# Performance work log

Hardware: AMD Instinct MI355X
Metric: run time of the kernel (lower is better)

## Reference

```python
import jax, jax.numpy as jnp
import numpy as np

N = 50000      # nodes
E = 800000     # edges
XS = 64        # x_size
ES = 32        # edge_attr dim (in_size = XS + ES = 96)
OUT = 64       # out_size
H = 128        # hidden_size
EPS = 1e-5


def _lin_init(k, fan_in, fan_out):
    s = 1.0 / np.sqrt(fan_in)
    kw, kb = jax.random.split(k)
    w = jax.random.uniform(kw, (fan_in, fan_out), minval=-s, maxval=s, dtype=jnp.float32)
    b = jax.random.uniform(kb, (fan_out,), minval=-s, maxval=s, dtype=jnp.float32)
    return w, b


def setup_inputs() -> dict:
    key = jax.random.key(0)
    ks = jax.random.split(key, 12)
    x = jax.random.normal(ks[0], (N, XS), dtype=jnp.float32)
    edge_index = jax.random.randint(ks[1], (2, E), 0, N, dtype=jnp.int64)
    edge_attr = jax.random.normal(ks[2], (E, ES), dtype=jnp.float32)
    u = jax.random.normal(ks[3], (1, 8), dtype=jnp.float32)
    batch = jnp.zeros((N,), dtype=jnp.int64)
    # MLP1: (96->128) LReLU (128->128) LReLU (128->64) LReLU LN(64)
    m1w0, m1b0 = _lin_init(ks[4], XS + ES, H)
    m1w1, m1b1 = _lin_init(ks[5], H, H)
    m1w2, m1b2 = _lin_init(ks[6], H, OUT)
    ln1_g = jnp.ones((OUT,), jnp.float32); ln1_b = jnp.zeros((OUT,), jnp.float32)
    # MLP2: (128->128) LReLU (128->128) LReLU (128->64) LReLU LN(64)
    m2w0, m2b0 = _lin_init(ks[7], XS + OUT, H)
    m2w1, m2b1 = _lin_init(ks[8], H, H)
    m2w2, m2b2 = _lin_init(ks[9], H, OUT)
    ln2_g = jnp.ones((OUT,), jnp.float32); ln2_b = jnp.zeros((OUT,), jnp.float32)
    return dict(x=x, edge_index=edge_index, edge_attr=edge_attr, u=u, batch=batch,
                m1w0=m1w0, m1b0=m1b0, m1w1=m1w1, m1b1=m1b1, m1w2=m1w2, m1b2=m1b2,
                ln1_g=ln1_g, ln1_b=ln1_b,
                m2w0=m2w0, m2b0=m2b0, m2w1=m2w1, m2b1=m2b1, m2w2=m2w2, m2b2=m2b2,
                ln2_g=ln2_g, ln2_b=ln2_b)


def _lrelu(v):
    return jax.nn.leaky_relu(v, 0.01)


def _layernorm(v, g, b):
    mu = jnp.mean(v, axis=-1, keepdims=True)
    var = jnp.mean(jnp.square(v - mu), axis=-1, keepdims=True)
    return (v - mu) * jax.lax.rsqrt(var + EPS) * g + b


def _mlp(h, w0, b0, w1, b1, w2, b2, g, bn):
    h = _lrelu(h @ w0 + b0)
    h = _lrelu(h @ w1 + b1)
    h = _lrelu(h @ w2 + b2)          # activate_last=True
    return _layernorm(h, g, bn)      # layer_norm=True


def reference(x, edge_index, edge_attr, u, batch,
              m1w0, m1b0, m1w1, m1b1, m1w2, m1b2, ln1_g, ln1_b,
              m2w0, m2b0, m2w1, m2b1, m2w2, m2b2, ln2_g, ln2_b):
    row, col = edge_index[0], edge_index[1]
    # gather source nodes, concat edge features -> per-edge MLP
    h = jnp.concatenate([x[row], edge_attr], axis=1)            # [E, 96]
    h = _mlp(h, m1w0, m1b0, m1w1, m1b1, m1w2, m1b2, ln1_g, ln1_b)  # [E, 64]
    # scatter_mean over destination nodes
    agg = jax.ops.segment_sum(h, col, num_segments=N)           # [N, 64]
    cnt = jax.ops.segment_sum(jnp.ones((E,), h.dtype), col, num_segments=N)
    agg = agg / jnp.maximum(cnt, 1.0)[:, None]
    # node update MLP
    h2 = jnp.concatenate([x, agg], axis=1)                      # [N, 128]
    return _mlp(h2, m2w0, m2b0, m2w1, m2b1, m2w2, m2b2, ln2_g, ln2_b)
```

## Files before the change

kernel.cpp:

```cpp
#include <hip/hip_runtime.h>


#define NNODES 50000
#define NEDGES 800000
#define NTILES_E2 3125
#define NTILES_N2 196

typedef __bf16 bf16;
typedef __bf16 __attribute__((ext_vector_type(4))) bf16x4;
typedef __bf16 __attribute__((ext_vector_type(8))) bf16x8;
typedef float __attribute__((ext_vector_type(4))) f32x4;

__device__ __forceinline__ f32x4 mfma_bf16(bf16x8 a, bf16x8 b, f32x4 c) {
    return __builtin_amdgcn_mfma_f32_16x16x32_bf16(a, b, c, 0, 0, 0);
}

__global__ void prep_weights(const float* __restrict__ w10, const float* __restrict__ w11,
                             const float* __restrict__ w12, const float* __restrict__ w20,
                             const float* __restrict__ w21, const float* __restrict__ w22,
                             bf16* __restrict__ img) {
    int idx = blockIdx.x * 256 + threadIdx.x;
    float f;
    if (idx < 13312) {
        int n = idx / 104, k = idx % 104;
        f = (k < 96) ? w10[k * 128 + n] : 0.0f;
    } else if (idx < 30720) {
        int t = idx - 13312; int n = t / 136, k = t % 136;
        f = (k < 128) ? w11[k * 128 + n] : 0.0f;
    } else if (idx < 39424) {
        int t = idx - 30720; int n = t / 136, k = t % 136;
        f = (k < 128) ? w12[k * 64 + n] : 0.0f;
    } else if (idx < 56832) {
        int t = idx - 39424; int n = t / 136, k = t % 136;
        f = (k < 128) ? w20[k * 128 + n] : 0.0f;
    } else if (idx < 74240) {
        int t = idx - 56832; int n = t / 136, k = t % 136;
        f = (k < 128) ? w21[k * 128 + n] : 0.0f;
    } else if (idx < 82944) {
        int t = idx - 74240; int n = t / 136, k = t % 136;
        f = (k < 128) ? w22[k * 64 + n] : 0.0f;
    } else {
        return;
    }
    img[idx] = (bf16)f;
}

__global__ void hist_kernel(const int* __restrict__ col, int* __restrict__ hist) {
    int i = blockIdx.x * 512 + threadIdx.x;
    if (i < NEDGES) {
        int d = col[i];
        if ((unsigned)d < (unsigned)NNODES) atomicAdd(hist + d, 1);
    }
}

__global__ void scanA(const int* __restrict__ hist, int* __restrict__ off,
                      int* __restrict__ csum) {
    __shared__ int sd[512];
    int t = threadIdx.x, i = blockIdx.x * 512 + t;
    int v = (i < NNODES) ? hist[i] : 0;
    sd[t] = v;
    __syncthreads();
    for (int o2 = 1; o2 < 512; o2 <<= 1) {
        int x = (t >= o2) ? sd[t - o2] : 0;
        __syncthreads();
        sd[t] += x;
        __syncthreads();
    }
    if (i < NNODES) off[i] = sd[t] - v;
    if (t == 511) csum[blockIdx.x] = sd[511];
}

__global__ void scanB(int* __restrict__ csum) {
    __shared__ int sd[128];
    int t = threadIdx.x;
    int v = (t < 98) ? csum[t] : 0;
    sd[t] = v;
    __syncthreads();
    for (int o2 = 1; o2 < 128; o2 <<= 1) {
        int x = (t >= o2) ? sd[t - o2] : 0;
        __syncthreads();
        sd[t] += x;
        __syncthreads();
    }
    if (t < 98) csum[t] = sd[t] - v;
}

__global__ void scanC(int* __restrict__ off, const int* __restrict__ csum) {
    int i = blockIdx.x * 512 + threadIdx.x;
    if (i < NNODES) off[i] += csum[blockIdx.x];
}

__global__ void scatter_kernel(const int* __restrict__ eidx, int* __restrict__ off,
                               int* __restrict__ perm, int* __restrict__ rdS) {
    int i = blockIdx.x * 512 + threadIdx.x;
    if (i < NEDGES) {
        int r = eidx[i], d = eidx[NEDGES + i];
        if ((unsigned)d < (unsigned)NNODES && (unsigned)r < (unsigned)NNODES) {
            int pos = atomicAdd(off + d, 1);
            if ((unsigned)pos < (unsigned)NEDGES) {
                perm[pos] = i;
                rdS[pos] = (int)(((unsigned)r & 0xFFFFu) | ((unsigned)d << 16));
            }
        }
    }
}

__global__ __launch_bounds__(512, 2) void edge_mlp(
    const float* __restrict__ x, const int* __restrict__ perm,
    const int* __restrict__ rdS, const float* __restrict__ eattr,
    const bf16* __restrict__ wimg,
    const float* __restrict__ b0g, const float* __restrict__ b1g,
    const float* __restrict__ b2g, const float* __restrict__ lng,
    const float* __restrict__ lnb, float* __restrict__ agg) {
    __shared__ __align__(16) bf16 wall[39424];
    __shared__ __align__(16) bf16 buf[256 * 136];
    __shared__ float bs[448];
    __shared__ int dstile[256];

    const int tid = threadIdx.x;
    {
        const uint4* src = (const uint4*)wimg;
        uint4* dst = (uint4*)wall;
        for (int i = tid; i < 4928; i += 512) dst[i] = src[i];
    }
    if (tid < 128) { bs[tid] = b0g[tid]; bs[128 + tid] = b1g[tid]; }
    else if (tid < 192) {
        int t = tid - 128;
        bs[256 + t] = b2g[t]; bs[320 + t] = lng[t]; bs[384 + t] = lnb[t];
    }
    __syncthreads();

    const int lane = tid & 63;
    const int wv = tid >> 6;
    const int col16 = lane & 15;
    const int quad = lane >> 4;

    float b0r[8], b1r[8], b2r[4], gr[4], br[4];
#pragma unroll
    for (int i = 0; i < 8; i++) { b0r[i] = bs[i * 16 + col16]; b1r[i] = bs[128 + i * 16 + col16]; }
#pragma unroll
    for (int i = 0; i < 4; i++) {
        b2r[i] = bs[256 + i * 16 + col16];
        gr[i] = bs[320 + i * 16 + col16];
        br[i] = bs[384 + i * 16 + col16];
    }

    const bf16* w0t = wall;
    const bf16* w1t = wall + 13312;
    const bf16* w2t = wall + 30720;

    const f32x4 vzero = {0.0f, 0.0f, 0.0f, 0.0f};
    const int r0 = wv * 32 + col16;
    const int rw = wv * 32 + quad * 4;
    const int el = tid >> 1, half = tid & 1;
    const int G = gridDim.x;

    int tile = blockIdx.x;

    float4 xr[8], er[4];
    unsigned cv;
    {
        int s = tile * 256 + el;
        cv = (unsigned)rdS[s];
        int ce = perm[s];
        int r = (int)(cv & 0xFFFFu); if (r >= NNODES) r = 0;
        if ((unsigned)ce >= (unsigned)NEDGES) ce = 0;
        const float4* xs = (const float4*)(x + (size_t)r * 64) + half * 8;
        const float4* es = (const float4*)(eattr + (size_t)ce * 32) + half * 4;
#pragma unroll
        for (int j = 0; j < 8; j++) xr[j] = xs[j];
#pragma unroll
        for (int j = 0; j < 4; j++) er[j] = es[j];
    }
    unsigned nv; int ne;
    {
        int t1 = tile + G;
        int s = (t1 < NTILES_E2 ? t1 * 256 : 0) + el;
        nv = (unsigned)rdS[s];
        ne = perm[s];
    }

    for (; tile < NTILES_E2; tile += G) {
        {
            unsigned d = cv >> 16;
            if (half == 0) dstile[el] = (d < (unsigned)NNODES) ? (int)d : 0;
            bf16* arow = buf + el * 136;
#pragma unroll
            for (int j = 0; j < 8; j++) {
                float4 vv = xr[j];
                bf16x4 u = {(bf16)vv.x, (bf16)vv.y, (bf16)vv.z, (bf16)vv.w};
                *(bf16x4*)(arow + half * 32 + j * 4) = u;
            }
#pragma unroll
            for (int j = 0; j < 4; j++) {
                float4 vv = er[j];
                bf16x4 u = {(bf16)vv.x, (bf16)vv.y, (bf16)vv.z, (bf16)vv.w};
                *(bf16x4*)(arow + 64 + half * 16 + j * 4) = u;
            }
        }
        __syncthreads();

        {
            int t2 = tile + G;
            if (t2 < NTILES_E2) {
                int r = (int)(nv & 0xFFFFu); if (r >= NNODES) r = 0;
                int e = ne; if ((unsigned)e >= (unsigned)NEDGES) e = 0;
                const float4* xs = (const float4*)(x + (size_t)r * 64) + half * 8;
                const float4* es = (const float4*)(eattr + (size_t)e * 32) + half * 4;
#pragma unroll
                for (int j = 0; j < 8; j++) xr[j] = xs[j];
#pragma unroll
                for (int j = 0; j < 4; j++) er[j] = es[j];
            }
        }
        unsigned pv; int pe;
        {
            int t3 = tile + 2 * G;
            int s = (t3 < NTILES_E2 ? t3 * 256 : 0) + el;
            pv = (unsigned)rdS[s];
            pe = perm[s];
        }

        f32x4 acc1[2][8];
#pragma unroll
        for (int mt = 0; mt < 2; mt++)
#pragma unroll
            for (int nt = 0; nt < 8; nt++) acc1[mt][nt] = vzero;
#pragma unroll
        for (int ks = 0; ks < 3; ks++) {
            bf16x8 a0 = *(const bf16x8*)(buf + r0 * 136 + ks * 32 + quad * 8);
            bf16x8 a1 = *(const bf16x8*)(buf + (r0 + 16) * 136 + ks * 32 + quad * 8);
#pragma unroll
            for (int nt = 0; nt < 8; nt++) {
                bf16x8 b = *(const bf16x8*)(w0t + (nt * 16 + col16) * 104 + ks * 32 + quad * 8);
                acc1[0][nt] = mfma_bf16(a0, b, acc1[0][nt]);
                acc1[1][nt] = mfma_bf16(a1, b, acc1[1][nt]);
            }
        }
#pragma unroll
        for (int mt = 0; mt < 2; mt++)
#pragma unroll
            for (int nt = 0; nt < 8; nt++)
#pragma unroll
                for (int rg = 0; rg < 4; rg++) {
                    float v = acc1[mt][nt][rg] + b0r[nt];
                    v = (v > 0.0f) ? v : 0.01f * v;
                    buf[(rw + mt * 16 + rg) * 136 + nt * 16 + col16] = (bf16)v;
                }

        bf16x8 a2[2][4];
#pragma unroll
        for (int mt = 0; mt < 2; mt++)
#pragma unroll
            for (int ks = 0; ks < 4; ks++)
                a2[mt][ks] = *(const bf16x8*)(buf + (r0 + mt * 16) * 136 + ks * 32 + quad * 8);
        f32x4 acc2[2][8];
#pragma unroll
        for (int mt = 0; mt < 2; mt++)
#pragma unroll
            for (int nt = 0; nt < 8; nt++) acc2[mt][nt] = vzero;
#pragma unroll
        for (int ks = 0; ks < 4; ks++) {
#pragma unroll
            for (int nt = 0; nt < 8; nt++) {
                bf16x8 b = *(const bf16x8*)(w1t + (nt * 16 + col16) * 136 + ks * 32 + quad * 8);
                acc2[0][nt] = mfma_bf16(a2[0][ks], b, acc2[0][nt]);
                acc2[1][nt] = mfma_bf16(a2[1][ks], b, acc2[1][nt]);
            }
        }
#pragma unroll
        for (int mt = 0; mt < 2; mt++)
#pragma unroll
            for (int nt = 0; nt < 8; nt++)
#pragma unroll
                for (int rg = 0; rg < 4; rg++) {
                    float v = acc2[mt][nt][rg] + b1r[nt];
                    v = (v > 0.0f) ? v : 0.01f * v;
                    buf[(rw + mt * 16 + rg) * 136 + nt * 16 + col16] = (bf16)v;
                }

        bf16x8 a3[2][4];
#pragma unroll
        for (int mt = 0; mt < 2; mt++)
#pragma unroll
            for (int ks = 0; ks < 4; ks++)
                a3[mt][ks] = *(const bf16x8*)(buf + (r0 + mt * 16) * 136 + ks * 32 + quad * 8);
        f32x4 acc3[2][4];
#pragma unroll
        for (int mt = 0; mt < 2; mt++)
#pragma unroll
            for (int nt = 0; nt < 4; nt++) acc3[mt][nt] = vzero;
#pragma unroll
        for (int ks = 0; ks < 4; ks++) {
#pragma unroll
            for (int nt = 0; nt < 4; nt++) {
                bf16x8 b = *(const bf16x8*)(w2t + (nt * 16 + col16) * 136 + ks * 32 + quad * 8);
                acc3[0][nt] = mfma_bf16(a3[0][ks], b, acc3[0][nt]);
                acc3[1][nt] = mfma_bf16(a3[1][ks], b, acc3[1][nt]);
            }
        }

        int drA[2][4];
#pragma unroll
        for (int mt = 0; mt < 2; mt++)
#pragma unroll
            for (int rg = 0; rg < 4; rg++) {
                int c = dstile[rw + mt * 16 + rg];
                drA[mt][rg] = ((unsigned)c < (unsigned)NNODES) ? c : 0;
            }
        __syncthreads();

#pragma unroll
        for (int mt = 0; mt < 2; mt++) {
            float vals[4][4];
            float s1[4] = {0.f, 0.f, 0.f, 0.f}, s2[4] = {0.f, 0.f, 0.f, 0.f};
#pragma unroll
            for (int nt = 0; nt < 4; nt++)
#pragma unroll
                for (int rg = 0; rg < 4; rg++) {
                    float v = acc3[mt][nt][rg] + b2r[nt];
                    v = (v > 0.0f) ? v : 0.01f * v;
                    vals[nt][rg] = v;
                    s1[rg] += v;
                    s2[rg] += v * v;
                }
#pragma unroll
            for (int off2 = 1; off2 < 16; off2 <<= 1) {
#pragma unroll
                for (int rg = 0; rg < 4; rg++) {
                    s1[rg] += __shfl_xor(s1[rg], off2);
                    s2[rg] += __shfl_xor(s2[rg], off2);
                }
            }
            float o[4][4];
#pragma unroll
            for (int rg = 0; rg < 4; rg++) {
                float mu = s1[rg] * 0.015625f;
                float var = s2[rg] * 0.015625f - mu * mu;
                float rstd = rsqrtf(var + 1e-5f);
#pragma unroll
                for (int nt = 0; nt < 4; nt++)
                    o[nt][rg] = (vals[nt][rg] - mu) * rstd * gr[nt] + br[nt];
            }
            float run0 = o[0][0], run1 = o[1][0], run2 = o[2][0], run3 = o[3][0];
            int cur = drA[mt][0];
#pragma unroll
            for (int rg = 1; rg < 4; rg++) {
                if (drA[mt][rg] != cur) {
                    float* dst = agg + (size_t)cur * 64 + col16;
                    atomicAdd(dst, run0); atomicAdd(dst + 16, run1);
                    atomicAdd(dst + 32, run2); atomicAdd(dst + 48, run3);
                    run0 = o[0][rg]; run1 = o[1][rg]; run2 = o[2][rg]; run3 = o[3][rg];
                    cur = drA[mt][rg];
                } else {
                    run0 += o[0][rg]; run1 += o[1][rg]; run2 += o[2][rg]; run3 += o[3][rg];
                }
            }
            float* dst = agg + (size_t)cur * 64 + col16;
            atomicAdd(dst, run0); atomicAdd(dst + 16, run1);
            atomicAdd(dst + 32, run2); atomicAdd(dst + 48, run3);
        }

        cv = nv; nv = pv; ne = pe;
    }
}

__global__ __launch_bounds__(512, 2) void node_mlp(
    const float* __restrict__ x, const float* __restrict__ agg,
    const int* __restrict__ hist, const bf16* __restrict__ wimg,
    const float* __restrict__ b0g, const float* __restrict__ b1g,
    const float* __restrict__ b2g, const float* __restrict__ lng,
    const float* __restrict__ lnb, float* __restrict__ out) {
    __shared__ __align__(16) bf16 wall[43520];
    __shared__ __align__(16) bf16 buf[256 * 136];
    __shared__ float bs[448];

    const int tid = threadIdx.x;
    {
        const uint4* src = (const uint4*)wimg;
        uint4* dst = (uint4*)wall;
        for (int i = tid; i < 5440; i += 512) dst[i] = src[i];
    }
    if (tid < 128) { bs[tid] = b0g[tid]; bs[128 + tid] = b1g[tid]; }
    else if (tid < 192) {
        int t = tid - 128;
        bs[256 + t] = b2g[t]; bs[320 + t] = lng[t]; bs[384 + t] = lnb[t];
    }
    __syncthreads();

    const int lane = tid & 63;
    const int wv = tid >> 6;
    const int col16 = lane & 15;
    const int quad = lane >> 4;

    float b0r[8], b1r[8], b2r[4], gr[4], br[4];
#pragma unroll
    for (int i = 0; i < 8; i++) { b0r[i] = bs[i * 16 + col16]; b1r[i] = bs[128 + i * 16 + col16]; }
#pragma unroll
    for (int i = 0; i < 4; i++) {
        b2r[i] = bs[256 + i * 16 + col16];
        gr[i] = bs[320 + i * 16 + col16];
        br[i] = bs[384 + i * 16 + col16];
    }

    const bf16* w0t = wall;
    const bf16* w1t = wall + 17408;
    const bf16* w2t = wall + 34816;

    const f32x4 vzero = {0.0f, 0.0f, 0.0f, 0.0f};
    const int r0 = wv * 32 + col16;
    const int rw = wv * 32 + quad * 4;
    const int el = tid >> 1, half = tid & 1;
    const int G = gridDim.x;

    int tile = blockIdx.x;
    if (tile >= NTILES_N2) return;

    float4 xr[8], ar[8];
    int cc;
    {
        int i = tile * 256 + el;
        if (i >= NNODES) i = NNODES - 1;
        const float4* xs = (const float4*)(x + (size_t)i * 64) + half * 8;
        const float4* as = (const float4*)(agg + (size_t)i * 64) + half * 8;
#pragma unroll
        for (int j = 0; j < 8; j++) { xr[j] = xs[j]; ar[j] = as[j]; }
        cc = hist[i];
    }

    for (; tile < NTILES_N2; tile += G) {
        const int nbase = tile * 256;
        {
            float inv = 1.0f / (float)(cc > 1 ? cc : 1);
            bf16* arow = buf + el * 136;
#pragma unroll
            for (int j = 0; j < 8; j++) {
                float4 v = xr[j];
                bf16x4 u = {(bf16)v.x, (bf16)v.y, (bf16)v.z, (bf16)v.w};
                *(bf16x4*)(arow + half * 32 + j * 4) = u;
            }
#pragma unroll
            for (int j = 0; j < 8; j++) {
                float4 v = ar[j];
                bf16x4 u = {(bf16)(v.x * inv), (bf16)(v.y * inv), (bf16)(v.z * inv), (bf16)(v.w * inv)};
                *(bf16x4*)(arow + 64 + half * 32 + j * 4) = u;
            }
        }
        __syncthreads();

        {
            int t2 = tile + G;
            if (t2 < NTILES_N2) {
                int i = t2 * 256 + el;
                if (i >= NNODES) i = NNODES - 1;
                const float4* xs = (const float4*)(x + (size_t)i * 64) + half * 8;
                const float4* as = (const float4*)(agg + (size_t)i * 64) + half * 8;
#pragma unroll
                for (int j = 0; j < 8; j++) { xr[j] = xs[j]; ar[j] = as[j]; }
                cc = hist[i];
            }
        }

        f32x4 acc1[2][8];
#pragma unroll
        for (int mt = 0; mt < 2; mt++)
#pragma unroll
            for (int nt = 0; nt < 8; nt++) acc1[mt][nt] = vzero;
#pragma unroll
        for (int ks = 0; ks < 4; ks++) {
            bf16x8 a0 = *(const bf16x8*)(buf + r0 * 136 + ks * 32 + quad * 8);
            bf16x8 a1 = *(const bf16x8*)(buf + (r0 + 16) * 136 + ks * 32 + quad * 8);
#pragma unroll
            for (int nt = 0; nt < 8; nt++) {
                bf16x8 b = *(const bf16x8*)(w0t + (nt * 16 + col16) * 136 + ks * 32 + quad * 8);
                acc1[0][nt] = mfma_bf16(a0, b, acc1[0][nt]);
                acc1[1][nt] = mfma_bf16(a1, b, acc1[1][nt]);
            }
        }
#pragma unroll
        for (int mt = 0; mt < 2; mt++)
#pragma unroll
            for (int nt = 0; nt < 8; nt++)
#pragma unroll
                for (int rg = 0; rg < 4; rg++) {
                    float v = acc1[mt][nt][rg] + b0r[nt];
                    v = (v > 0.0f) ? v : 0.01f * v;
                    buf[(rw + mt * 16 + rg) * 136 + nt * 16 + col16] = (bf16)v;
                }

        bf16x8 a2[2][4];
#pragma unroll
        for (int mt = 0; mt < 2; mt++)
#pragma unroll
            for (int ks = 0; ks < 4; ks++)
                a2[mt][ks] = *(const bf16x8*)(buf + (r0 + mt * 16) * 136 + ks * 32 + quad * 8);
        f32x4 acc2[2][8];
#pragma unroll
        for (int mt = 0; mt < 2; mt++)
#pragma unroll
            for (int nt = 0; nt < 8; nt++) acc2[mt][nt] = vzero;
#pragma unroll
        for (int ks = 0; ks < 4; ks++) {
#pragma unroll
            for (int nt = 0; nt < 8; nt++) {
                bf16x8 b = *(const bf16x8*)(w1t + (nt * 16 + col16) * 136 + ks * 32 + quad * 8);
                acc2[0][nt] = mfma_bf16(a2[0][ks], b, acc2[0][nt]);
                acc2[1][nt] = mfma_bf16(a2[1][ks], b, acc2[1][nt]);
            }
        }
#pragma unroll
        for (int mt = 0; mt < 2; mt++)
#pragma unroll
            for (int nt = 0; nt < 8; nt++)
#pragma unroll
                for (int rg = 0; rg < 4; rg++) {
                    float v = acc2[mt][nt][rg] + b1r[nt];
                    v = (v > 0.0f) ? v : 0.01f * v;
                    buf[(rw + mt * 16 + rg) * 136 + nt * 16 + col16] = (bf16)v;
                }

        bf16x8 a3[2][4];
#pragma unroll
        for (int mt = 0; mt < 2; mt++)
#pragma unroll
            for (int ks = 0; ks < 4; ks++)
                a3[mt][ks] = *(const bf16x8*)(buf + (r0 + mt * 16) * 136 + ks * 32 + quad * 8);
        f32x4 acc3[2][4];
#pragma unroll
        for (int mt = 0; mt < 2; mt++)
#pragma unroll
            for (int nt = 0; nt < 4; nt++) acc3[mt][nt] = vzero;
#pragma unroll
        for (int ks = 0; ks < 4; ks++) {
#pragma unroll
            for (int nt = 0; nt < 4; nt++) {
                bf16x8 b = *(const bf16x8*)(w2t + (nt * 16 + col16) * 136 + ks * 32 + quad * 8);
                acc3[0][nt] = mfma_bf16(a3[0][ks], b, acc3[0][nt]);
                acc3[1][nt] = mfma_bf16(a3[1][ks], b, acc3[1][nt]);
            }
        }
        __syncthreads();

#pragma unroll
        for (int mt = 0; mt < 2; mt++) {
            float vals[4][4];
            float s1[4] = {0.f, 0.f, 0.f, 0.f}, s2[4] = {0.f, 0.f, 0.f, 0.f};
#pragma unroll
            for (int nt = 0; nt < 4; nt++)
#pragma unroll
                for (int rg = 0; rg < 4; rg++) {
                    float v = acc3[mt][nt][rg] + b2r[nt];
                    v = (v > 0.0f) ? v : 0.01f * v;
                    vals[nt][rg] = v;
                    s1[rg] += v;
                    s2[rg] += v * v;
                }
#pragma unroll
            for (int off2 = 1; off2 < 16; off2 <<= 1) {
#pragma unroll
                for (int rg = 0; rg < 4; rg++) {
                    s1[rg] += __shfl_xor(s1[rg], off2);
                    s2[rg] += __shfl_xor(s2[rg], off2);
                }
            }
#pragma unroll
            for (int rg = 0; rg < 4; rg++) {
                float mu = s1[rg] * 0.015625f;
                float var = s2[rg] * 0.015625f - mu * mu;
                float rstd = rsqrtf(var + 1e-5f);
                int i = nbase + rw + mt * 16 + rg;
                if (i < NNODES) {
#pragma unroll
                    for (int nt = 0; nt < 4; nt++) {
                        float o = (vals[nt][rg] - mu) * rstd * gr[nt] + br[nt];
                        out[(size_t)i * 64 + nt * 16 + col16] = o;
                    }
                }
            }
        }
    }
}

extern "C" void kernel_launch(void* const* d_in, const int* in_sizes, int n_in,
                              void* d_out, int out_size, void* d_ws, size_t ws_size,
                              hipStream_t stream) {
    (void)in_sizes; (void)n_in; (void)out_size; (void)ws_size;
    const float* x     = (const float*)d_in[0];
    const int*   eidx  = (const int*)d_in[1];
    const float* eattr = (const float*)d_in[2];
    const float* m1w0 = (const float*)d_in[5];
    const float* m1b0 = (const float*)d_in[6];
    const float* m1w1 = (const float*)d_in[7];
    const float* m1b1 = (const float*)d_in[8];
    const float* m1w2 = (const float*)d_in[9];
    const float* m1b2 = (const float*)d_in[10];
    const float* ln1g = (const float*)d_in[11];
    const float* ln1b = (const float*)d_in[12];
    const float* m2w0 = (const float*)d_in[13];
    const float* m2b0 = (const float*)d_in[14];
    const float* m2w1 = (const float*)d_in[15];
    const float* m2b1 = (const float*)d_in[16];
    const float* m2w2 = (const float*)d_in[17];
    const float* m2b2 = (const float*)d_in[18];
    const float* ln2g = (const float*)d_in[19];
    const float* ln2b = (const float*)d_in[20];

    char* ws = (char*)d_ws;
    float* agg  = (float*)ws;
    int*   hist = (int*)(ws + 12800000);
    int*   off  = (int*)(ws + 13000000);
    int*   csum = (int*)(ws + 13200000);
    int*   perm = (int*)(ws + 13200512);
    int*   rdS  = (int*)(ws + 16400512);
    bf16*  wimg = (bf16*)(ws + 19600512);

    hipMemsetAsync(d_ws, 0, 13000000, stream);
    prep_weights<<<324, 256, 0, stream>>>(m1w0, m1w1, m1w2, m2w0, m2w1, m2w2, wimg);
    hist_kernel<<<1563, 512, 0, stream>>>(eidx + NEDGES, hist);
    scanA<<<98, 512, 0, stream>>>(hist, off, csum);
    scanB<<<1, 128, 0, stream>>>(csum);
    scanC<<<98, 512, 0, stream>>>(off, csum);
    scatter_kernel<<<1563, 512, 0, stream>>>(eidx, off, perm, rdS);
    edge_mlp<<<256, 512, 0, stream>>>(x, perm, rdS, eattr, wimg, m1b0, m1b1, m1b2,
                                      ln1g, ln1b, agg);
    node_mlp<<<196, 512, 0, stream>>>(x, agg, hist, wimg + 39424,
                                      m2b0, m2b1, m2b2, ln2g, ln2b, (float*)d_out);
}
```

Before: 489.6 us.

## Fuse all stages into one persistent cooperative kernel with grid syncs

Replaces the memset, weight prep, histogram, three-stage scan, scatter, edge MLP and node MLP launches with a single cooperative kernel of 256 blocks that separates phases with grid-wide syncs. Zeroing and weight conversion now run inside the kernel, and the scan's second pass is replaced by each block summing the preceding block totals. This removes per-launch overhead and gaps between the many small kernels. In exchange it adds several grid barriers, runs the small phases with only 256 blocks, and the node MLP must now share one larger LDS allocation and launch configuration with the edge phase.

New measurement: 942.3 us. 92.5% more time.

```diff
diff --git a/kernel.cpp b/kernel.cpp
--- a/kernel.cpp
+++ b/kernel.cpp
@@ -1,10 +1,15 @@
 #include <hip/hip_runtime.h>
+#include <hip/hip_cooperative_groups.h>
+
+namespace cg = cooperative_groups;
 
 
 #define NNODES 50000
 #define NEDGES 800000
-#define NTILES_E2 3125
-#define NTILES_N2 196
+#define NTILES_E 3125
+#define NTILES_N 196
+#define GRID 256
+#define TPB 512
 
 typedef __bf16 bf16;
 typedef __bf16 __attribute__((ext_vector_type(4))) bf16x4;
@@ -15,85 +20,104 @@
     return __builtin_amdgcn_mfma_f32_16x16x32_bf16(a, b, c, 0, 0, 0);
 }
 
-__global__ void prep_weights(const float* __restrict__ w10, const float* __restrict__ w11,
-                             const float* __restrict__ w12, const float* __restrict__ w20,
-                             const float* __restrict__ w21, const float* __restrict__ w22,
-                             bf16* __restrict__ img) {
-    int idx = blockIdx.x * 256 + threadIdx.x;
-    float f;
-    if (idx < 13312) {
-        int n = idx / 104, k = idx % 104;
-        f = (k < 96) ? w10[k * 128 + n] : 0.0f;
-    } else if (idx < 30720) {
-        int t = idx - 13312; int n = t / 136, k = t % 136;
-        f = (k < 128) ? w11[k * 128 + n] : 0.0f;
-    } else if (idx < 39424) {
-        int t = idx - 30720; int n = t / 136, k = t % 136;
-        f = (k < 128) ? w12[k * 64 + n] : 0.0f;
-    } else if (idx < 56832) {
-        int t = idx - 39424; int n = t / 136, k = t % 136;
-        f = (k < 128) ? w20[k * 128 + n] : 0.0f;
-    } else if (idx < 74240) {
-        int t = idx - 56832; int n = t / 136, k = t % 136;
-        f = (k < 128) ? w21[k * 128 + n] : 0.0f;
-    } else if (idx < 82944) {
-        int t = idx - 74240; int n = t / 136, k = t % 136;
-        f = (k < 128) ? w22[k * 64 + n] : 0.0f;
-    } else {
-        return;
-    }
-    img[idx] = (bf16)f;
-}
-
-__global__ void hist_kernel(const int* __restrict__ col, int* __restrict__ hist) {
-    int i = blockIdx.x * 512 + threadIdx.x;
-    if (i < NEDGES) {
-        int d = col[i];
+__global__ __launch_bounds__(TPB) void fused_gnn(
+    const float* __restrict__ x, const int* __restrict__ eidx,
+    const float* __restrict__ eattr,
+    const float* __restrict__ w10, const float* __restrict__ w11,
+    const float* __restrict__ w12, const float* __restrict__ w20,
+    const float* __restrict__ w21, const float* __restrict__ w22,
+    const float* __restrict__ b10, const float* __restrict__ b11,
+    const float* __restrict__ b12, const float* __restrict__ l1g,
+    const float* __restrict__ l1b,
+    const float* __restrict__ b20, const float* __restrict__ b21,
+    const float* __restrict__ b22, const float* __restrict__ l2g,
+    const float* __restrict__ l2b,
+    float* __restrict__ out, char* __restrict__ ws) {
+    cg::grid_group gg = cg::this_grid();
+
+    float* agg  = (float*)ws;
+    int*   hist = (int*)(ws + 12800000);
+    int*   off  = (int*)(ws + 13000000);
+    int*   csum = (int*)(ws + 13200000);
+    int*   perm = (int*)(ws + 13200512);
+    int*   rdS  = (int*)(ws + 16400512);
+    bf16*  wimg = (bf16*)(ws + 19600512);
+
+    __shared__ __align__(16) bf16 wall[43520];
+    __shared__ __align__(16) bf16 buf[256 * 136];
+    __shared__ float bs[448];
+    __shared__ int dstile[256];
+
+    const int tid = threadIdx.x;
+    const int gtid = blockIdx.x * TPB + tid;
+    const int gstride = GRID * TPB;
+
+    for (int i = gtid; i < 3250000; i += gstride) ((int*)ws)[i] = 0;
+    for (int idx = gtid; idx < 82944; idx += gstride) {
+        float f;
+        if (idx < 13312)      { int n = idx / 104, k = idx % 104; f = (k < 96) ? w10[k * 128 + n] : 0.0f; }
+        else if (idx < 30720) { int t2 = idx - 13312; int n = t2 / 136, k = t2 % 136; f = (k < 128) ? w11[k * 128 + n] : 0.0f; }
+        else if (idx < 39424) { int t2 = idx - 30720; int n = t2 / 136, k = t2 % 136; f = (k < 128) ? w12[k * 64 + n] : 0.0f; }
+        else if (idx < 56832) { int t2 = idx - 39424; int n = t2 / 136, k = t2 % 136; f = (k < 128) ? w20[k * 128 + n] : 0.0f; }
+        else if (idx < 74240) { int t2 = idx - 56832; int n = t2 / 136, k = t2 % 136; f = (k < 128) ? w21[k * 128 + n] : 0.0f; }
+        else                  { int t2 = idx - 74240; int n = t2 / 136, k = t2 % 136; f = (k < 128) ? w22[k * 64 + n] : 0.0f; }
+        wimg[idx] = (bf16)f;
+    }
+    __threadfence();
+    gg.sync();
+
+    {
+        const uint4* src = (const uint4*)wimg;
+        uint4* dst = (uint4*)wall;
+        for (int i = tid; i < 4928; i += TPB) dst[i] = src[i];
+    }
+    if (tid < 128) { bs[tid] = b10[tid]; bs[128 + tid] = b11[tid]; }
+    else if (tid < 192) {
+        int t2 = tid - 128;
+        bs[256 + t2] = b12[t2]; bs[320 + t2] = l1g[t2]; bs[384 + t2] = l1b[t2];
+    }
+    for (int i = gtid; i < NEDGES; i += gstride) {
+        int d = eidx[NEDGES + i];
         if ((unsigned)d < (unsigned)NNODES) atomicAdd(hist + d, 1);
     }
-}
-
-__global__ void scanA(const int* __restrict__ hist, int* __restrict__ off,
-                      int* __restrict__ csum) {
-    __shared__ int sd[512];
-    int t = threadIdx.x, i = blockIdx.x * 512 + t;
-    int v = (i < NNODES) ? hist[i] : 0;
-    sd[t] = v;
-    __syncthreads();
-    for (int o2 = 1; o2 < 512; o2 <<= 1) {
-        int x = (t >= o2) ? sd[t - o2] : 0;
+    __threadfence();
+    gg.sync();
+
+    if (blockIdx.x < 98) {
+        int* sd = (int*)buf;
+        int i = blockIdx.x * 512 + tid;
+        int v = (i < NNODES) ? hist[i] : 0;
+        sd[tid] = v;
         __syncthreads();
-        sd[t] += x;
+        for (int o2 = 1; o2 < 512; o2 <<= 1) {
+            int xv = (tid >= o2) ? sd[tid - o2] : 0;
+            __syncthreads();
+            sd[tid] += xv;
+            __syncthreads();
+        }
+        if (i < NNODES) off[i] = sd[tid] - v;
+        if (tid == 511) csum[blockIdx.x] = sd[511];
+    }
+    __threadfence();
+    gg.sync();
+
+    if (blockIdx.x < 98) {
+        if (tid < 64) {
+            int p = 0;
+            for (int j = tid; j < (int)blockIdx.x; j += 64) p += csum[j];
+#pragma unroll
+            for (int o = 32; o > 0; o >>= 1) p += __shfl_down(p, o);
+            if (tid == 0) dstile[0] = p;
+        }
         __syncthreads();
-    }
-    if (i < NNODES) off[i] = sd[t] - v;
-    if (t == 511) csum[blockIdx.x] = sd[511];
-}
-
-__global__ void scanB(int* __restrict__ csum) {
-    __shared__ int sd[128];
-    int t = threadIdx.x;
-    int v = (t < 98) ? csum[t] : 0;
-    sd[t] = v;
-    __syncthreads();
-    for (int o2 = 1; o2 < 128; o2 <<= 1) {
-        int x = (t >= o2) ? sd[t - o2] : 0;
-        __syncthreads();
-        sd[t] += x;
-        __syncthreads();
-    }
-    if (t < 98) csum[t] = sd[t] - v;
-}
-
-__global__ void scanC(int* __restrict__ off, const int* __restrict__ csum) {
-    int i = blockIdx.x * 512 + threadIdx.x;
-    if (i < NNODES) off[i] += csum[blockIdx.x];
-}
-
-__global__ void scatter_kernel(const int* __restrict__ eidx, int* __restrict__ off,
-                               int* __restrict__ perm, int* __restrict__ rdS) {
-    int i = blockIdx.x * 512 + threadIdx.x;
-    if (i < NEDGES) {
+        int pre = dstile[0];
+        int i = blockIdx.x * 512 + tid;
+        if (i < NNODES) off[i] += pre;
+    }
+    __threadfence();
+    gg.sync();
+
+    for (int i = gtid; i < NEDGES; i += gstride) {
         int r = eidx[i], d = eidx[NEDGES + i];
         if ((unsigned)d < (unsigned)NNODES && (unsigned)r < (unsigned)NNODES) {
             int pos = atomicAdd(off + d, 1);
@@ -103,477 +127,408 @@
             }
         }
     }
-}
-
-__global__ __launch_bounds__(512, 2) void edge_mlp(
-    const float* __restrict__ x, const int* __restrict__ perm,
-    const int* __restrict__ rdS, const float* __restrict__ eattr,
-    const bf16* __restrict__ wimg,
-    const float* __restrict__ b0g, const float* __restrict__ b1g,
-    const float* __restrict__ b2g, const float* __restrict__ lng,
-    const float* __restrict__ lnb, float* __restrict__ agg) {
-    __shared__ __align__(16) bf16 wall[39424];
-    __shared__ __align__(16) bf16 buf[256 * 136];
-    __shared__ float bs[448];
-    __shared__ int dstile[256];
-
-    const int tid = threadIdx.x;
-    {
-        const uint4* src = (const uint4*)wimg;
-        uint4* dst = (uint4*)wall;
-        for (int i = tid; i < 4928; i += 512) dst[i] = src[i];
-    }
-    if (tid < 128) { bs[tid] = b0g[tid]; bs[128 + tid] = b1g[tid]; }
-    else if (tid < 192) {
-        int t = tid - 128;
-        bs[256 + t] = b2g[t]; bs[320 + t] = lng[t]; bs[384 + t] = lnb[t];
-    }
-    __syncthreads();
+    __threadfence();
+    gg.sync();
 
     const int lane = tid & 63;
     const int wv = tid >> 6;
     const int col16 = lane & 15;
     const int quad = lane >> 4;
-
-    float b0r[8], b1r[8], b2r[4], gr[4], br[4];
-#pragma unroll
-    for (int i = 0; i < 8; i++) { b0r[i] = bs[i * 16 + col16]; b1r[i] = bs[128 + i * 16 + col16]; }
-#pragma unroll
-    for (int i = 0; i < 4; i++) {
-        b2r[i] = bs[256 + i * 16 + col16];
-        gr[i] = bs[320 + i * 16 + col16];
-        br[i] = bs[384 + i * 16 + col16];
-    }
-
-    const bf16* w0t = wall;
-    const bf16* w1t = wall + 13312;
-    const bf16* w2t = wall + 30720;
-
+    const int el = tid >> 1, half = tid & 1;
     const f32x4 vzero = {0.0f, 0.0f, 0.0f, 0.0f};
-    const int r0 = wv * 32 + col16;
-    const int rw = wv * 32 + quad * 4;
-    const int el = tid >> 1, half = tid & 1;
-    const int G = gridDim.x;
-
-    int tile = blockIdx.x;
-
-    float4 xr[8], er[4];
-    unsigned cv;
     {
-        int s = tile * 256 + el;
-        cv = (unsigned)rdS[s];
-        int ce = perm[s];
-        int r = (int)(cv & 0xFFFFu); if (r >= NNODES) r = 0;
-        if ((unsigned)ce >= (unsigned)NEDGES) ce = 0;
-        const float4* xs = (const float4*)(x + (size_t)r * 64) + half * 8;
-        const float4* es = (const float4*)(eattr + (size_t)ce * 32) + half * 4;
-#pragma unroll
-        for (int j = 0; j < 8; j++) xr[j] = xs[j];
-#pragma unroll
-        for (int j = 0; j < 4; j++) er[j] = es[j];
-    }
-    unsigned nv; int ne;
+        float b0r[8], b1r[8], b2r[4], gr[4], br[4];
+#pragma unroll
+        for (int i = 0; i < 8; i++) { b0r[i] = bs[i * 16 + col16]; b1r[i] = bs[128 + i * 16 + col16]; }
+#pragma unroll
+        for (int i = 0; i < 4; i++) {
+            b2r[i] = bs[256 + i * 16 + col16];
+            gr[i] = bs[320 + i * 16 + col16];
+            br[i] = bs[384 + i * 16 + col16];
+        }
+        const bf16* w0t = wall;
+        const bf16* w1t = wall + 13312;
+        const bf16* w2t = wall + 30720;
+        const int r0 = wv * 32 + col16;
+        const int rw = wv * 32 + quad * 4;
+
+        int tile = blockIdx.x;
+        float4 xr[8], er[4];
+        unsigned cv;
+        {
+            int s = tile * 256 + el;
+            cv = (unsigned)rdS[s];
+            int ce = perm[s];
+            int r = (int)(cv & 0xFFFFu); if (r >= NNODES) r = 0;
+            if ((unsigned)ce >= (unsigned)NEDGES) ce = 0;
+            const float4* xs = (const float4*)(x + (size_t)r * 64) + half * 8;
+            const float4* es = (const float4*)(eattr + (size_t)ce * 32) + half * 4;
+#pragma unroll
+            for (int j = 0; j < 8; j++) xr[j] = xs[j];
+#pragma unroll
+            for (int j = 0; j < 4; j++) er[j] = es[j];
+        }
+        unsigned nv; int ne;
+        {
+            int t1 = tile + GRID;
+            int s = (t1 < NTILES_E ? t1 * 256 : 0) + el;
+            nv = (unsigned)rdS[s];
+            ne = perm[s];
+        }
+
+        for (; tile < NTILES_E; tile += GRID) {
+            {
+                unsigned d = cv >> 16;
+                if (half == 0) dstile[el] = (d < (unsigned)NNODES) ? (int)d : 0;
+                bf16* arow = buf + el * 136;
+#pragma unroll
+                for (int j = 0; j < 8; j++) {
+                    float4 vv = xr[j];
+                    bf16x4 u = {(bf16)vv.x, (bf16)vv.y, (bf16)vv.z, (bf16)vv.w};
+                    *(bf16x4*)(arow + half * 32 + j * 4) = u;
+                }
+#pragma unroll
+                for (int j = 0; j < 4; j++) {
+                    float4 vv = er[j];
+                    bf16x4 u = {(bf16)vv.x, (bf16)vv.y, (bf16)vv.z, (bf16)vv.w};
+                    *(bf16x4*)(arow + 64 + half * 16 + j * 4) = u;
+                }
+            }
+            __syncthreads();
+
+            {
+                int t2 = tile + GRID;
+                if (t2 < NTILES_E) {
+                    int r = (int)(nv & 0xFFFFu); if (r >= NNODES) r = 0;
+                    int e = ne; if ((unsigned)e >= (unsigned)NEDGES) e = 0;
+                    const float4* xs = (const float4*)(x + (size_t)r * 64) + half * 8;
+                    const float4* es = (const float4*)(eattr + (size_t)e * 32) + half * 4;
+#pragma unroll
+                    for (int j = 0; j < 8; j++) xr[j] = xs[j];
+#pragma unroll
+                    for (int j = 0; j < 4; j++) er[j] = es[j];
+                }
+            }
+            unsigned pv; int pe;
+            {
+                int t3 = tile + 2 * GRID;
+                int s = (t3 < NTILES_E ? t3 * 256 : 0) + el;
+                pv = (unsigned)rdS[s];
+                pe = perm[s];
+            }
+
+            f32x4 acc1[2][8];
+#pragma unroll
+            for (int mt = 0; mt < 2; mt++)
+#pragma unroll
+                for (int nt = 0; nt < 8; nt++) acc1[mt][nt] = vzero;
+#pragma unroll
+            for (int ks = 0; ks < 3; ks++) {
+                bf16x8 a0 = *(const bf16x8*)(buf + r0 * 136 + ks * 32 + quad * 8);
+                bf16x8 a1 = *(const bf16x8*)(buf + (r0 + 16) * 136 + ks * 32 + quad * 8);
+#pragma unroll
+                for (int nt = 0; nt < 8; nt++) {
+                    bf16x8 b = *(const bf16x8*)(w0t + (nt * 16 + col16) * 104 + ks * 32 + quad * 8);
+                    acc1[0][nt] = mfma_bf16(a0, b, acc1[0][nt]);
+                    acc1[1][nt] = mfma_bf16(a1, b, acc1[1][nt]);
+                }
+            }
+#pragma unroll
+            for (int mt = 0; mt < 2; mt++)
+#pragma unroll
+                for (int nt = 0; nt < 8; nt++)
+#pragma unroll
+                    for (int rg = 0; rg < 4; rg++) {
+                        float v = acc1[mt][nt][rg] + b0r[nt];
+                        v = (v > 0.0f) ? v : 0.01f * v;
+                        buf[(rw + mt * 16 + rg) * 136 + nt * 16 + col16] = (bf16)v;
+                    }
+
+            bf16x8 a2[2][4];
+#pragma unroll
+            for (int mt = 0; mt < 2; mt++)
+#pragma unroll
+                for (int ks = 0; ks < 4; ks++)
+                    a2[mt][ks] = *(const bf16x8*)(buf + (r0 + mt * 16) * 136 + ks * 32 + quad * 8);
+            f32x4 acc2[2][8];
+#pragma unroll
+            for (int mt = 0; mt < 2; mt++)
+#pragma unroll
+                for (int nt = 0; nt < 8; nt++) acc2[mt][nt] = vzero;
+#pragma unroll
+            for (int ks = 0; ks < 4; ks++) {
+#pragma unroll
+                for (int nt = 0; nt < 8; nt++) {
+                    bf16x8 b = *(const bf16x8*)(w1t + (nt * 16 + col16) * 136 + ks * 32 + quad * 8);
+                    acc2[0][nt] = mfma_bf16(a2[0][ks], b, acc2[0][nt]);
+                    acc2[1][nt] = mfma_bf16(a2[1][ks], b, acc2[1][nt]);
+                }
+            }
+#pragma unroll
+            for (int mt = 0; mt < 2; mt++)
+#pragma unroll
+                for (int nt = 0; nt < 8; nt++)
+#pragma unroll
+                    for (int rg = 0; rg < 4; rg++) {
+                        float v = acc2[mt][nt][rg] + b1r[nt];
+                        v = (v > 0.0f) ? v : 0.01f * v;
+                        buf[(rw + mt * 16 + rg) * 136 + nt * 16 + col16] = (bf16)v;
+                    }
+
+            bf16x8 a3[2][4];
+#pragma unroll
+            for (int mt = 0; mt < 2; mt++)
+#pragma unroll
+                for (int ks = 0; ks < 4; ks++)
+                    a3[mt][ks] = *(const bf16x8*)(buf + (r0 + mt * 16) * 136 + ks * 32 + quad * 8);
+            f32x4 acc3[2][4];
+#pragma unroll
+            for (int mt = 0; mt < 2; mt++)
+#pragma unroll
+                for (int nt = 0; nt < 4; nt++) acc3[mt][nt] = vzero;
+#pragma unroll
+            for (int ks = 0; ks < 4; ks++) {
+#pragma unroll
+                for (int nt = 0; nt < 4; nt++) {
+                    bf16x8 b = *(const bf16x8*)(w2t + (nt * 16 + col16) * 136 + ks * 32 + quad * 8);
+                    acc3[0][nt] = mfma_bf16(a3[0][ks], b, acc3[0][nt]);
+                    acc3[1][nt] = mfma_bf16(a3[1][ks], b, acc3[1][nt]);
+                }
+            }
+
+            int drA[2][4];
+#pragma unroll
+            for (int mt = 0; mt < 2; mt++)
+#pragma unroll
+                for (int rg = 0; rg < 4; rg++) {
+                    int c = dstile[rw + mt * 16 + rg];
+                    drA[mt][rg] = ((unsigned)c < (unsigned)NNODES) ? c : 0;
+                }
+            __syncthreads();
+
+#pragma unroll
+            for (int mt = 0; mt < 2; mt++) {
+                float vals[4][4];
+                float s1[4] = {0.f, 0.f, 0.f, 0.f}, s2[4] = {0.f, 0.f, 0.f, 0.f};
+#pragma unroll
+                for (int nt = 0; nt < 4; nt++)
+#pragma unroll
+                    for (int rg = 0; rg < 4; rg++) {
+                        float v = acc3[mt][nt][rg] + b2r[nt];
+                        v = (v > 0.0f) ? v : 0.01f * v;
+                        vals[nt][rg] = v;
+                        s1[rg] += v;
+                        s2[rg] += v * v;
+                    }
+#pragma unroll
+                for (int off2 = 1; off2 < 16; off2 <<= 1) {
+#pragma unroll
+                    for (int rg = 0; rg < 4; rg++) {
+                        s1[rg] += __shfl_xor(s1[rg], off2);
+                        s2[rg] += __shfl_xor(s2[rg], off2);
+                    }
+                }
+                float o[4][4];
+#pragma unroll
+                for (int rg = 0; rg < 4; rg++) {
+                    float mu = s1[rg] * 0.015625f;
+                    float var = s2[rg] * 0.015625f - mu * mu;
+                    float rstd = rsqrtf(var + 1e-5f);
+#pragma unroll
+                    for (int nt = 0; nt < 4; nt++)
+                        o[nt][rg] = (vals[nt][rg] - mu) * rstd * gr[nt] + br[nt];
+                }
+                float run0 = o[0][0], run1 = o[1][0], run2 = o[2][0], run3 = o[3][0];
+                int cur = drA[mt][0];
+#pragma unroll
+                for (int rg = 1; rg < 4; rg++) {
+                    if (drA[mt][rg] != cur) {
+                        float* dst = agg + (size_t)cur * 64 + col16;
+                        atomicAdd(dst, run0); atomicAdd(dst + 16, run1);
+                        atomicAdd(dst + 32, run2); atomicAdd(dst + 48, run3);
+                        run0 = o[0][rg]; run1 = o[1][rg]; run2 = o[2][rg]; run3 = o[3][rg];
+                        cur = drA[mt][rg];
+                    } else {
+                        run0 += o[0][rg]; run1 += o[1][rg]; run2 += o[2][rg]; run3 += o[3][rg];
+                    }
+                }
+                float* dst = agg + (size_t)cur * 64 + col16;
+                atomicAdd(dst, run0); atomicAdd(dst + 16, run1);
+                atomicAdd(dst + 32, run2); atomicAdd(dst + 48, run3);
+            }
+
+            cv = nv; nv = pv; ne = pe;
+        }
+    }
+    __threadfence();
+    gg.sync();
+
     {
-        int t1 = tile + G;
-        int s = (t1 < NTILES_E2 ? t1 * 256 : 0) + el;
-        nv = (unsigned)rdS[s];
-        ne = perm[s];
-    }
-
-    for (; tile < NTILES_E2; tile += G) {
-        {
-            unsigned d = cv >> 16;
-            if (half == 0) dstile[el] = (d < (unsigned)NNODES) ? (int)d : 0;
-            bf16* arow = buf + el * 136;
-#pragma unroll
-            for (int j = 0; j < 8; j++) {
-                float4 vv = xr[j];
-                bf16x4 u = {(bf16)vv.x, (bf16)vv.y, (bf16)vv.z, (bf16)vv.w};
-                *(bf16x4*)(arow + half * 32 + j * 4) = u;
-            }
-#pragma unroll
-            for (int j = 0; j < 4; j++) {
-                float4 vv = er[j];
-                bf16x4 u = {(bf16)vv.x, (bf16)vv.y, (bf16)vv.z, (bf16)vv.w};
-                *(bf16x4*)(arow + 64 + half * 16 + j * 4) = u;
-            }
-        }
-        __syncthreads();
-
-        {
-            int t2 = tile + G;
-            if (t2 < NTILES_E2) {
-                int r = (int)(nv & 0xFFFFu); if (r >= NNODES) r = 0;
-                int e = ne; if ((unsigned)e >= (unsigned)NEDGES) e = 0;
-                const float4* xs = (const float4*)(x + (size_t)r * 64) + half * 8;
-                const float4* es = (const float4*)(eattr + (size_t)e * 32) + half * 4;
-#pragma unroll
-                for (int j = 0; j < 8; j++) xr[j] = xs[j];
-#pragma unroll
-                for (int j = 0; j < 4; j++) er[j] = es[j];
-            }
-        }
-        unsigned pv; int pe;
-        {
-            int t3 = tile + 2 * G;
-            int s = (t3 < NTILES_E2 ? t3 * 256 : 0) + el;
-            pv = (unsigned)rdS[s];
-            pe = perm[s];
-        }
-
-        f32x4 acc1[2][8];
-#pragma unroll
-        for (int mt = 0; mt < 2; mt++)
-#pragma unroll
-            for (int nt = 0; nt < 8; nt++) acc1[mt][nt] = vzero;
-#pragma unroll
-        for (int ks = 0; ks < 3; ks++) {
-            bf16x8 a0 = *(const bf16x8*)(buf + r0 * 136 + ks * 32 + quad * 8);
-            bf16x8 a1 = *(const bf16x8*)(buf + (r0 + 16) * 136 + ks * 32 + quad * 8);
-#pragma unroll
-            for (int nt = 0; nt < 8; nt++) {
-                bf16x8 b = *(const bf16x8*)(w0t + (nt * 16 + col16) * 104 + ks * 32 + quad * 8);
-                acc1[0][nt] = mfma_bf16(a0, b, acc1[0][nt]);
-                acc1[1][nt] = mfma_bf16(a1, b, acc1[1][nt]);
-            }
-        }
-#pragma unroll
-        for (int mt = 0; mt < 2; mt++)
-#pragma unroll
-            for (int nt = 0; nt < 8; nt++)
-#pragma unroll
-                for (int rg = 0; rg < 4; rg++) {
-                    float v = acc1[mt][nt][rg] + b0r[nt];
-                    v = (v > 0.0f) ? v : 0.01f * v;
-                    buf[(rw + mt * 16 + rg) * 136 + nt * 16 + col16] = (bf16)v;
-                }
-
-        bf16x8 a2[2][4];
-#pragma unroll
-        for (int mt = 0; mt < 2; mt++)
-#pragma unroll
-            for (int ks = 0; ks < 4; ks++)
-                a2[mt][ks] = *(const bf16x8*)(buf + (r0 + mt * 16) * 136 + ks * 32 + quad * 8);
-        f32x4 acc2[2][8];
-#pragma unroll
-        for (int mt = 0; mt < 2; mt++)
-#pragma unroll
-            for (int nt = 0; nt < 8; nt++) acc2[mt][nt] = vzero;
-#pragma unroll
-        for (int ks = 0; ks < 4; ks++) {
-#pragma unroll
-            for (int nt = 0; nt < 8; nt++) {
-                bf16x8 b = *(const bf16x8*)(w1t + (nt * 16 + col16) * 136 + ks * 32 + quad * 8);
-                acc2[0][nt] = mfma_bf16(a2[0][ks], b, acc2[0][nt]);
-                acc2[1][nt] = mfma_bf16(a2[1][ks], b, acc2[1][nt]);
-            }
-        }
-#pragma unroll
-        for (int mt = 0; mt < 2; mt++)
-#pragma unroll
-            for (int nt = 0; nt < 8; nt++)
-#pragma unroll
-                for (int rg = 0; rg < 4; rg++) {
-                    float v = acc2[mt][nt][rg] + b1r[nt];
-                    v = (v > 0.0f) ? v : 0.01f * v;
-                    buf[(rw + mt * 16 + rg) * 136 + nt * 16 + col16] = (bf16)v;
-                }
-
-        bf16x8 a3[2][4];
-#pragma unroll
-        for (int mt = 0; mt < 2; mt++)
-#pragma unroll
-            for (int ks = 0; ks < 4; ks++)
-                a3[mt][ks] = *(const bf16x8*)(buf + (r0 + mt * 16) * 136 + ks * 32 + quad * 8);
-        f32x4 acc3[2][4];
-#pragma unroll
-        for (int mt = 0; mt < 2; mt++)
-#pragma unroll
-            for (int nt = 0; nt < 4; nt++) acc3[mt][nt] = vzero;
-#pragma unroll
-        for (int ks = 0; ks < 4; ks++) {
-#pragma unroll
-            for (int nt = 0; nt < 4; nt++) {
-                bf16x8 b = *(const bf16x8*)(w2t + (nt * 16 + col16) * 136 + ks * 32 + quad * 8);
-                acc3[0][nt] = mfma_bf16(a3[0][ks], b, acc3[0][nt]);
-                acc3[1][nt] = mfma_bf16(a3[1][ks], b, acc3[1][nt]);
-            }
-        }
-
-        int drA[2][4];
-#pragma unroll
-        for (int mt = 0; mt < 2; mt++)
-#pragma unroll
-            for (int rg = 0; rg < 4; rg++) {
-                int c = dstile[rw + mt * 16 + rg];
-                drA[mt][rg] = ((unsigned)c < (unsigned)NNODES) ? c : 0;
-            }
-        __syncthreads();
-
-#pragma unroll
-        for (int mt = 0; mt < 2; mt++) {
-            float vals[4][4];
-            float s1[4] = {0.f, 0.f, 0.f, 0.f}, s2[4] = {0.f, 0.f, 0.f, 0.f};
-#pragma unroll
-            for (int nt = 0; nt < 4; nt++)
-#pragma unroll
-                for (int rg = 0; rg < 4; rg++) {
-                    float v = acc3[mt][nt][rg] + b2r[nt];
-                    v = (v > 0.0f) ? v : 0.01f * v;
-                    vals[nt][rg] = v;
-                    s1[rg] += v;
-                    s2[rg] += v * v;
-                }
-#pragma unroll
-            for (int off2 = 1; off2 < 16; off2 <<= 1) {
-#pragma unroll
-                for (int rg = 0; rg < 4; rg++) {
-                    s1[rg] += __shfl_xor(s1[rg], off2);
-                    s2[rg] += __shfl_xor(s2[rg], off2);
-                }
-            }
-            float o[4][4];
-#pragma unroll
-            for (int rg = 0; rg < 4; rg++) {
-                float mu = s1[rg] * 0.015625f;
-                float var = s2[rg] * 0.015625f - mu * mu;
-                float rstd = rsqrtf(var + 1e-5f);
-#pragma unroll
-                for (int nt = 0; nt < 4; nt++)
-                    o[nt][rg] = (vals[nt][rg] - mu) * rstd * gr[nt] + br[nt];
-            }
-            float run0 = o[0][0], run1 = o[1][0], run2 = o[2][0], run3 = o[3][0];
-            int cur = drA[mt][0];
-#pragma unroll
-            for (int rg = 1; rg < 4; rg++) {
-                if (drA[mt][rg] != cur) {
-                    float* dst = agg + (size_t)cur * 64 + col16;
-                    atomicAdd(dst, run0); atomicAdd(dst + 16, run1);
-                    atomicAdd(dst + 32, run2); atomicAdd(dst + 48, run3);
-                    run0 = o[0][rg]; run1 = o[1][rg]; run2 = o[2][rg]; run3 = o[3][rg];
-                    cur = drA[mt][rg];
-                } else {
-                    run0 += o[0][rg]; run1 += o[1][rg]; run2 += o[2][rg]; run3 += o[3][rg];
-                }
-            }
-            float* dst = agg + (size_t)cur * 64 + col16;
-            atomicAdd(dst, run0); atomicAdd(dst + 16, run1);
-            atomicAdd(dst + 32, run2); atomicAdd(dst + 48, run3);
-        }
-
-        cv = nv; nv = pv; ne = pe;
-    }
-}
-
-__global__ __launch_bounds__(512, 2) void node_mlp(
-    const float* __restrict__ x, const float* __restrict__ agg,
-    const int* __restrict__ hist, const bf16* __restrict__ wimg,
-    const float* __restrict__ b0g, const float* __restrict__ b1g,
-    const float* __restrict__ b2g, const float* __restrict__ lng,
-    const float* __restrict__ lnb, float* __restrict__ out) {
-    __shared__ __align__(16) bf16 wall[43520];
-    __shared__ __align__(16) bf16 buf[256 * 136];
-    __shared__ float bs[448];
-
-    const int tid = threadIdx.x;
+        const uint4* src = (const uint4*)(wimg + 39424);
+        uint4* dst = (uint4*)wall;
+        for (int i = tid; i < 5440; i += TPB) dst[i] = src[i];
+    }
+    if (tid < 128) { bs[tid] = b20[tid]; bs[128 + tid] = b21[tid]; }
+    else if (tid < 192) {
+        int t2 = tid - 128;
+        bs[256 + t2] = b22[t2]; bs[320 + t2] = l2g[t2]; bs[384 + t2] = l2b[t2];
+    }
+    __syncthreads();
     {
-        const uint4* src = (const uint4*)wimg;
-        uint4* dst = (uint4*)wall;
-        for (int i = tid; i < 5440; i += 512) dst[i] = src[i];
-    }
-    if (tid < 128) { bs[tid] = b0g[tid]; bs[128 + tid] = b1g[tid]; }
-    else if (tid < 192) {
-        int t = tid - 128;
-        bs[256 + t] = b2g[t]; bs[320 + t] = lng[t]; bs[384 + t] = lnb[t];
-    }
-    __syncthreads();
-
-    const int lane = tid & 63;
-    const int wv = tid >> 6;
-    const int col16 = lane & 15;
-    const int quad = lane >> 4;
-
-    float b0r[8], b1r[8], b2r[4], gr[4], br[4];
-#pragma unroll
-    for (int i = 0; i < 8; i++) { b0r[i] = bs[i * 16 + col16]; b1r[i] = bs[128 + i * 16 + col16]; }
-#pragma unroll
-    for (int i = 0; i < 4; i++) {
-        b2r[i] = bs[256 + i * 16 + col16];
-        gr[i] = bs[320 + i * 16 + col16];
-        br[i] = bs[384 + i * 16 + col16];
-    }
-
-    const bf16* w0t = wall;
-    const bf16* w1t = wall + 17408;
-    const bf16* w2t = wall + 34816;
-
-    const f32x4 vzero = {0.0f, 0.0f, 0.0f, 0.0f};
-    const int r0 = wv * 32 + col16;
-    const int rw = wv * 32 + quad * 4;
-    const int el = tid >> 1, half = tid & 1;
-    const int G = gridDim.x;
-
-    int tile = blockIdx.x;
-    if (tile >= NTILES_N2) return;
-
-    float4 xr[8], ar[8];
-    int cc;
-    {
-        int i = tile * 256 + el;
-        if (i >= NNODES) i = NNODES - 1;
-        const float4* xs = (const float4*)(x + (size_t)i * 64) + half * 8;
-        const float4* as = (const float4*)(agg + (size_t)i * 64) + half * 8;
-#pragma unroll
-        for (int j = 0; j < 8; j++) { xr[j] = xs[j]; ar[j] = as[j]; }
-        cc = hist[i];
-    }
-
-    for (; tile < NTILES_N2; tile += G) {
-        const int nbase = tile * 256;
-        {
-            float inv = 1.0f / (float)(cc > 1 ? cc : 1);
-            bf16* arow = buf + el * 136;
-#pragma unroll
-            for (int j = 0; j < 8; j++) {
-                float4 v = xr[j];
-                bf16x4 u = {(bf16)v.x, (bf16)v.y, (bf16)v.z, (bf16)v.w};
-                *(bf16x4*)(arow + half * 32 + j * 4) = u;
-            }
-#pragma unroll
-            for (int j = 0; j < 8; j++) {
-                float4 v = ar[j];
-                bf16x4 u = {(bf16)(v.x * inv), (bf16)(v.y * inv), (bf16)(v.z * inv), (bf16)(v.w * inv)};
-                *(bf16x4*)(arow + 64 + half * 32 + j * 4) = u;
-            }
-        }
-        __syncthreads();
-
-        {
-            int t2 = tile + G;
-            if (t2 < NTILES_N2) {
-                int i = t2 * 256 + el;
+        float b0r[8], b1r[8], b2r[4], gr[4], br[4];
+#pragma unroll
+        for (int i = 0; i < 8; i++) { b0r[i] = bs[i * 16 + col16]; b1r[i] = bs[128 + i * 16 + col16]; }
+#pragma unroll
+        for (int i = 0; i < 4; i++) {
+            b2r[i] = bs[256 + i * 16 + col16];
+            gr[i] = bs[320 + i * 16 + col16];
+            br[i] = bs[384 + i * 16 + col16];
+        }
+        const bf16* w0t = wall;
+        const bf16* w1t = wall + 17408;
+        const bf16* w2t = wall + 34816;
+        const int r0 = wv * 32 + col16;
+        const int rw = wv * 32 + quad * 4;
+
+        for (int tile = blockIdx.x; tile < NTILES_N; tile += GRID) {
+            const int nbase = tile * 256;
+            {
+                int i = nbase + el;
                 if (i >= NNODES) i = NNODES - 1;
                 const float4* xs = (const float4*)(x + (size_t)i * 64) + half * 8;
                 const float4* as = (const float4*)(agg + (size_t)i * 64) + half * 8;
-#pragma unroll
-                for (int j = 0; j < 8; j++) { xr[j] = xs[j]; ar[j] = as[j]; }
-                cc = hist[i];
-            }
-        }
-
-        f32x4 acc1[2][8];
-#pragma unroll
-        for (int mt = 0; mt < 2; mt++)
-#pragma unroll
-            for (int nt = 0; nt < 8; nt++) acc1[mt][nt] = vzero;
-#pragma unroll
-        for (int ks = 0; ks < 4; ks++) {
-            bf16x8 a0 = *(const bf16x8*)(buf + r0 * 136 + ks * 32 + quad * 8);
-            bf16x8 a1 = *(const bf16x8*)(buf + (r0 + 16) * 136 + ks * 32 + quad * 8);
-#pragma unroll
-            for (int nt = 0; nt < 8; nt++) {
-                bf16x8 b = *(const bf16x8*)(w0t + (nt * 16 + col16) * 136 + ks * 32 + quad * 8);
-                acc1[0][nt] = mfma_bf16(a0, b, acc1[0][nt]);
-                acc1[1][nt] = mfma_bf16(a1, b, acc1[1][nt]);
-            }
-        }
-#pragma unroll
-        for (int mt = 0; mt < 2; mt++)
-#pragma unroll
-            for (int nt = 0; nt < 8; nt++)
+                int c = hist[i];
+                float inv = 1.0f / (float)(c > 1 ? c : 1);
+                bf16* arow = buf + el * 136;
+#pragma unroll
+                for (int j = 0; j < 8; j++) {
+                    float4 v = xs[j];
+                    bf16x4 u = {(bf16)v.x, (bf16)v.y, (bf16)v.z, (bf16)v.w};
+                    *(bf16x4*)(arow + half * 32 + j * 4) = u;
+                }
+#pragma unroll
+                for (int j = 0; j < 8; j++) {
+                    float4 v = as[j];
+                    bf16x4 u = {(bf16)(v.x * inv), (bf16)(v.y * inv), (bf16)(v.z * inv), (bf16)(v.w * inv)};
+                    *(bf16x4*)(arow + 64 + half * 32 + j * 4) = u;
+                }
+            }
+            __syncthreads();
+
+            f32x4 acc1[2][8];
+#pragma unroll
+            for (int mt = 0; mt < 2; mt++)
+#pragma unroll
+                for (int nt = 0; nt < 8; nt++) acc1[mt][nt] = vzero;
+#pragma unroll
+            for (int ks = 0; ks < 4; ks++) {
+                bf16x8 a0 = *(const bf16x8*)(buf + r0 * 136 + ks * 32 + quad * 8);
+                bf16x8 a1 = *(const bf16x8*)(buf + (r0 + 16) * 136 + ks * 32 + quad * 8);
+#pragma unroll
+                for (int nt = 0; nt < 8; nt++) {
+                    bf16x8 b = *(const bf16x8*)(w0t + (nt * 16 + col16) * 136 + ks * 32 + quad * 8);
+                    acc1[0][nt] = mfma_bf16(a0, b, acc1[0][nt]);
+                    acc1[1][nt] = mfma_bf16(a1, b, acc1[1][nt]);
+                }
+            }
+#pragma unroll
+            for (int mt = 0; mt < 2; mt++)
+#pragma unroll
+                for (int nt = 0; nt < 8; nt++)
+#pragma unroll
+                    for (int rg = 0; rg < 4; rg++) {
+                        float v = acc1[mt][nt][rg] + b0r[nt];
+                        v = (v > 0.0f) ? v : 0.01f * v;
+                        buf[(rw + mt * 16 + rg) * 136 + nt * 16 + col16] = (bf16)v;
+                    }
+
+            bf16x8 a2[2][4];
+#pragma unroll
+            for (int mt = 0; mt < 2; mt++)
+#pragma unroll
+                for (int ks = 0; ks < 4; ks++)
+                    a2[mt][ks] = *(const bf16x8*)(buf + (r0 + mt * 16) * 136 + ks * 32 + quad * 8);
+            f32x4 acc2[2][8];
+#pragma unroll
+            for (int mt = 0; mt < 2; mt++)
+#pragma unroll
+                for (int nt = 0; nt < 8; nt++) acc2[mt][nt] = vzero;
+#pragma unroll
+            for (int ks = 0; ks < 4; ks++) {
+#pragma unroll
+                for (int nt = 0; nt < 8; nt++) {
+                    bf16x8 b = *(const bf16x8*)(w1t + (nt * 16 + col16) * 136 + ks * 32 + quad * 8);
+                    acc2[0][nt] = mfma_bf16(a2[0][ks], b, acc2[0][nt]);
+                    acc2[1][nt] = mfma_bf16(a2[1][ks], b, acc2[1][nt]);
+                }
+            }
+#pragma unroll
+            for (int mt = 0; mt < 2; mt++)
+#pragma unroll
+                for (int nt = 0; nt < 8; nt++)
+#pragma unroll
+                    for (int rg = 0; rg < 4; rg++) {
+                        float v = acc2[mt][nt][rg] + b1r[nt];
+                        v = (v > 0.0f) ? v : 0.01f * v;
+                        buf[(rw + mt * 16 + rg) * 136 + nt * 16 + col16] = (bf16)v;
+                    }
+
+            bf16x8 a3[2][4];
+#pragma unroll
+            for (int mt = 0; mt < 2; mt++)
+#pragma unroll
+                for (int ks = 0; ks < 4; ks++)
+                    a3[mt][ks] = *(const bf16x8*)(buf + (r0 + mt * 16) * 136 + ks * 32 + quad * 8);
+            f32x4 acc3[2][4];
+#pragma unroll
+            for (int mt = 0; mt < 2; mt++)
+#pragma unroll
+                for (int nt = 0; nt < 4; nt++) acc3[mt][nt] = vzero;
+#pragma unroll
+            for (int ks = 0; ks < 4; ks++) {
+#pragma unroll
+                for (int nt = 0; nt < 4; nt++) {
+                    bf16x8 b = *(const bf16x8*)(w2t + (nt * 16 + col16) * 136 + ks * 32 + quad * 8);
+                    acc3[0][nt] = mfma_bf16(a3[0][ks], b, acc3[0][nt]);
+                    acc3[1][nt] = mfma_bf16(a3[1][ks], b, acc3[1][nt]);
+                }
+            }
+            __syncthreads();
+
+#pragma unroll
+            for (int mt = 0; mt < 2; mt++) {
+                float vals[4][4];
+                float s1[4] = {0.f, 0.f, 0.f, 0.f}, s2[4] = {0.f, 0.f, 0.f, 0.f};
+#pragma unroll
+                for (int nt = 0; nt < 4; nt++)
+#pragma unroll
+                    for (int rg = 0; rg < 4; rg++) {
+                        float v = acc3[mt][nt][rg] + b2r[nt];
+                        v = (v > 0.0f) ? v : 0.01f * v;
+                        vals[nt][rg] = v;
+                        s1[rg] += v;
+                        s2[rg] += v * v;
+                    }
+#pragma unroll
+                for (int off2 = 1; off2 < 16; off2 <<= 1) {
+#pragma unroll
+                    for (int rg = 0; rg < 4; rg++) {
+                        s1[rg] += __shfl_xor(s1[rg], off2);
+                        s2[rg] += __shfl_xor(s2[rg], off2);
+                    }
+                }
 #pragma unroll
                 for (int rg = 0; rg < 4; rg++) {
-                    float v = acc1[mt][nt][rg] + b0r[nt];
-                    v = (v > 0.0f) ? v : 0.01f * v;
-                    buf[(rw + mt * 16 + rg) * 136 + nt * 16 + col16] = (bf16)v;
-                }
-
-        bf16x8 a2[2][4];
-#pragma unroll
-        for (int mt = 0; mt < 2; mt++)
-#pragma unroll
-            for (int ks = 0; ks < 4; ks++)
-                a2[mt][ks] = *(const bf16x8*)(buf + (r0 + mt * 16) * 136 + ks * 32 + quad * 8);
-        f32x4 acc2[2][8];
-#pragma unroll
-        for (int mt = 0; mt < 2; mt++)
-#pragma unroll
-            for (int nt = 0; nt < 8; nt++) acc2[mt][nt] = vzero;
-#pragma unroll
-        for (int ks = 0; ks < 4; ks++) {
-#pragma unroll
-            for (int nt = 0; nt < 8; nt++) {
-                bf16x8 b = *(const bf16x8*)(w1t + (nt * 16 + col16) * 136 + ks * 32 + quad * 8);
-                acc2[0][nt] = mfma_bf16(a2[0][ks], b, acc2[0][nt]);
-                acc2[1][nt] = mfma_bf16(a2[1][ks], b, acc2[1][nt]);
-            }
-        }
-#pragma unroll
-        for (int mt = 0; mt < 2; mt++)
-#pragma unroll
-            for (int nt = 0; nt < 8; nt++)
-#pragma unroll
-                for (int rg = 0; rg < 4; rg++) {
-                    float v = acc2[mt][nt][rg] + b1r[nt];
-                    v = (v > 0.0f) ? v : 0.01f * v;
-                    buf[(rw + mt * 16 + rg) * 136 + nt * 16 + col16] = (bf16)v;
-                }
-
-        bf16x8 a3[2][4];
-#pragma unroll
-        for (int mt = 0; mt < 2; mt++)
-#pragma unroll
-            for (int ks = 0; ks < 4; ks++)
-                a3[mt][ks] = *(const bf16x8*)(buf + (r0 + mt * 16) * 136 + ks * 32 + quad * 8);
-        f32x4 acc3[2][4];
-#pragma unroll
-        for (int mt = 0; mt < 2; mt++)
-#pragma unroll
-            for (int nt = 0; nt < 4; nt++) acc3[mt][nt] = vzero;
-#pragma unroll
-        for (int ks = 0; ks < 4; ks++) {
-#pragma unroll
-            for (int nt = 0; nt < 4; nt++) {
-                bf16x8 b = *(const bf16x8*)(w2t + (nt * 16 + col16) * 136 + ks * 32 + quad * 8);
-                acc3[0][nt] = mfma_bf16(a3[0][ks], b, acc3[0][nt]);
-                acc3[1][nt] = mfma_bf16(a3[1][ks], b, acc3[1][nt]);
-            }
-        }
-        __syncthreads();
-
-#pragma unroll
-        for (int mt = 0; mt < 2; mt++) {
-            float vals[4][4];
-            float s1[4] = {0.f, 0.f, 0.f, 0.f}, s2[4] = {0.f, 0.f, 0.f, 0.f};
-#pragma unroll
-            for (int nt = 0; nt < 4; nt++)
-#pragma unroll
-                for (int rg = 0; rg < 4; rg++) {
-                    float v = acc3[mt][nt][rg] + b2r[nt];
-                    v = (v > 0.0f) ? v : 0.01f * v;
-                    vals[nt][rg] = v;
-                    s1[rg] += v;
-                    s2[rg] += v * v;
-                }
-#pragma unroll
-            for (int off2 = 1; off2 < 16; off2 <<= 1) {
-#pragma unroll
-                for (int rg = 0; rg < 4; rg++) {
-                    s1[rg] += __shfl_xor(s1[rg], off2);
-                    s2[rg] += __shfl_xor(s2[rg], off2);
-                }
-            }
-#pragma unroll
-            for (int rg = 0; rg < 4; rg++) {
-                float mu = s1[rg] * 0.015625f;
-                float var = s2[rg] * 0.015625f - mu * mu;
-                float rstd = rsqrtf(var + 1e-5f);
-                int i = nbase + rw + mt * 16 + rg;
-                if (i < NNODES) {
-#pragma unroll
-                    for (int nt = 0; nt < 4; nt++) {
-                        float o = (vals[nt][rg] - mu) * rstd * gr[nt] + br[nt];
-                        out[(size_t)i * 64 + nt * 16 + col16] = o;
+                    float mu = s1[rg] * 0.015625f;
+                    float var = s2[rg] * 0.015625f - mu * mu;
+                    float rstd = rsqrtf(var + 1e-5f);
+                    int i = nbase + rw + mt * 16 + rg;
+                    if (i < NNODES) {
+#pragma unroll
+                        for (int nt = 0; nt < 4; nt++) {
+                            float o = (vals[nt][rg] - mu) * rstd * gr[nt] + br[nt];
+                            out[(size_t)i * 64 + nt * 16 + col16] = o;
+                        }
                     }
                 }
             }
@@ -604,25 +559,17 @@
     const float* m2b2 = (const float*)d_in[18];
     const float* ln2g = (const float*)d_in[19];
     const float* ln2b = (const float*)d_in[20];
-
+    float* outp = (float*)d_out;
     char* ws = (char*)d_ws;
-    float* agg  = (float*)ws;
-    int*   hist = (int*)(ws + 12800000);
-    int*   off  = (int*)(ws + 13000000);
-    int*   csum = (int*)(ws + 13200000);
-    int*   perm = (int*)(ws + 13200512);
-    int*   rdS  = (int*)(ws + 16400512);
-    bf16*  wimg = (bf16*)(ws + 19600512);
-
-    hipMemsetAsync(d_ws, 0, 13000000, stream);
-    prep_weights<<<324, 256, 0, stream>>>(m1w0, m1w1, m1w2, m2w0, m2w1, m2w2, wimg);
-    hist_kernel<<<1563, 512, 0, stream>>>(eidx + NEDGES, hist);
-    scanA<<<98, 512, 0, stream>>>(hist, off, csum);
-    scanB<<<1, 128, 0, stream>>>(csum);
-    scanC<<<98, 512, 0, stream>>>(off, csum);
-    scatter_kernel<<<1563, 512, 0, stream>>>(eidx, off, perm, rdS);
-    edge_mlp<<<256, 512, 0, stream>>>(x, perm, rdS, eattr, wimg, m1b0, m1b1, m1b2,
-                                      ln1g, ln1b, agg);
-    node_mlp<<<196, 512, 0, stream>>>(x, agg, hist, wimg + 39424,
-                                      m2b0, m2b1, m2b2, ln2g, ln2b, (float*)d_out);
+
+    void* args[] = {
+        (void*)&x, (void*)&eidx, (void*)&eattr,
+        (void*)&m1w0, (void*)&m1w1, (void*)&m1w2,
+        (void*)&m2w0, (void*)&m2w1, (void*)&m2w2,
+        (void*)&m1b0, (void*)&m1b1, (void*)&m1b2, (void*)&ln1g, (void*)&ln1b,
+        (void*)&m2b0, (void*)&m2b1, (void*)&m2b2, (void*)&ln2g, (void*)&ln2b,
+        (void*)&outp, (void*)&ws
+    };
+    hipLaunchCooperativeKernel((const void*)fused_gnn, dim3(GRID), dim3(TPB),
+                               args, 0, stream);
 }
```
